# Kernel optimization log

Measured on AMD Instinct MI355X. Metric: run time of the kernel, lower is better.

## Reference

```python
import jax, jax.numpy as jnp
import numpy as np

N_EL = 1024
N_UP = 512
D_EMB = 256
WIDTH = 64

def get_all_pair_indices(n_el, n_up):
    # static numpy precompute, identical to the source module
    ii, jj = np.meshgrid(np.arange(n_el), np.arange(n_el), indexing='ij')
    spin = np.concatenate([np.zeros(n_up, dtype=int), np.ones(n_el - n_up, dtype=int)])
    idx = np.stack([ii.flatten(), jj.flatten()], axis=0)
    idx = idx[:, idx[0] != idx[1]]
    same = spin[idx[0]] == spin[idx[1]]
    return idx[:, same], idx[:, ~same]

_PAIRS = get_all_pair_indices(N_EL, N_UP)

def logscaled_diff_features(diff):
    # [P,3] diff -> [P,4]: log-rescaled diff vector + log1p(distance)
    r = jnp.linalg.norm(diff, axis=-1, keepdims=True)
    return jnp.concatenate([diff * jnp.log1p(r) / r, jnp.log1p(r)], axis=-1)

def mlp3(x, W0, b0, W1, b1, W2, b2=None):
    h = jnp.tanh(x @ W0 + b0)
    h = jnp.tanh(h @ W1 + b1)
    out = h @ W2
    return out if b2 is None else out + b2

def _forward(electrons, embeddings, A_same, A_diff, Ws0_same, bs0_same, Ws1_same, bs1_same, Ws2_same, Ws0_diff, bs0_diff, Ws1_diff, bs1_diff, Ws2_diff, scale_same, scale_diff, We0, be0, We1, be1, We2, be2, mlp_scale, log_bias):
    (ics, ins_), (icd, ind_) = _PAIRS
    diff_same = electrons[ics] - electrons[ins_]   # [P_same,3]
    diff_diff = electrons[icd] - electrons[ind_]   # [P_diff,3]
    dist_same = jnp.linalg.norm(diff_same, axis=-1)
    dist_diff = jnp.linalg.norm(diff_diff, axis=-1)
    # Yukawa e-e cusp
    A_s = jax.nn.softplus(A_same); F_s = jnp.sqrt(2 * A_s)
    A_d = jax.nn.softplus(A_diff); F_d = jnp.sqrt(2 * A_d)
    logpsi = A_s * jnp.sum(jnp.expm1(-dist_same / F_s) / dist_same)
    logpsi = logpsi + A_d * jnp.sum(jnp.expm1(-dist_diff / F_d) / dist_diff)
    # pairwise e-e MLPs
    fs = logscaled_diff_features(diff_same)
    fd = logscaled_diff_features(diff_diff)
    logpsi = logpsi + jnp.sum(mlp3(fs, Ws0_same, bs0_same, Ws1_same, bs1_same, Ws2_same)) * scale_same
    logpsi = logpsi + jnp.sum(mlp3(fd, Ws0_diff, bs0_diff, Ws1_diff, bs1_diff, Ws2_diff)) * scale_diff
    # per-electron embedding MLP jastrow
    J = mlp3(embeddings, We0, be0, We1, be1, We2, be2) * mlp_scale  # [n_el, 2]
    J = J + jnp.stack([jnp.zeros(()), log_bias])
    jastrows = J.sum(axis=0)  # (2,)
    log_J = jastrows[1]
    sign = jnp.sign(log_J)
    logpsi = logpsi + jastrows[0] + jnp.log(jnp.abs(log_J))
    return sign, logpsi

def setup_inputs():
    key = jax.random.key(0)
    ks = jax.random.split(key, 16)
    rn = lambda k, s: jax.random.normal(k, s, dtype=jnp.float32)
    return dict(
        electrons=rn(ks[0], (N_EL, 3)),
        embeddings=rn(ks[1], (N_EL, D_EMB)),
        A_same=jnp.ones(()), A_diff=jnp.ones(()),
        Ws0_same=rn(ks[2], (4, WIDTH)) * 0.3, bs0_same=jnp.zeros((WIDTH,)),
        Ws1_same=rn(ks[3], (WIDTH, WIDTH)) * 0.1, bs1_same=jnp.zeros((WIDTH,)),
        Ws2_same=rn(ks[4], (WIDTH, 1)) * 0.1,
        Ws0_diff=rn(ks[5], (4, WIDTH)) * 0.3, bs0_diff=jnp.zeros((WIDTH,)),
        Ws1_diff=rn(ks[6], (WIDTH, WIDTH)) * 0.1, bs1_diff=jnp.zeros((WIDTH,)),
        Ws2_diff=rn(ks[7], (WIDTH, 1)) * 0.1,
        scale_same=rn(ks[8], ()) * 0.1, scale_diff=rn(ks[9], ()) * 0.1,
        We0=rn(ks[10], (D_EMB, WIDTH)) * 0.05, be0=jnp.zeros((WIDTH,)),
        We1=rn(ks[11], (WIDTH, WIDTH)) * 0.1, be1=jnp.zeros((WIDTH,)),
        We2=rn(ks[12], (WIDTH, 2)) * 0.1, be2=jnp.zeros((2,)),
        mlp_scale=rn(ks[13], (2,)) * 0.1,
        log_bias=jnp.ones(()),
    )

def reference(electrons, embeddings, A_same, A_diff, Ws0_same, bs0_same, Ws1_same, bs1_same, Ws2_same, Ws0_diff, bs0_diff, Ws1_diff, bs1_diff, Ws2_diff, scale_same, scale_diff, We0, be0, We1, be1, We2, be2, mlp_scale, log_bias):
    return _forward(electrons, embeddings, A_same, A_diff, Ws0_same, bs0_same, Ws1_same, bs1_same, Ws2_same, Ws0_diff, bs0_diff, Ws1_diff, bs1_diff, Ws2_diff, scale_same, scale_diff, We0, be0, We1, be1, We2, be2, mlp_scale, log_bias)
```

## Files before the change

kernel.cpp:

```cpp
#include <hip/hip_runtime.h>

#define NEL 1024
#define NUP 512
#define DEMB 256
#define WID 64

typedef __attribute__((ext_vector_type(4))) float f32x4;
typedef __attribute__((ext_vector_type(16))) float f32x16;
typedef __attribute__((ext_vector_type(4))) unsigned int u32x4;
typedef __attribute__((ext_vector_type(8))) _Float16 f16x8;
typedef __attribute__((ext_vector_type(2))) _Float16 h2;

#define CTANH 2.8853900817779268f
#define LOG2E 1.4426950408889634f
#define LN2   0.6931471805599453f


__device__ __forceinline__ float tanh_pre(float y) {
    float e = __builtin_amdgcn_exp2f(y);
    return fmaf(-2.0f, __builtin_amdgcn_rcpf(e + 1.0f), 1.0f);
}

__device__ __forceinline__ float softplus_f(float x) {
    return fmaxf(x, 0.0f) + __logf(1.0f + __expf(-fabsf(x)));
}

__device__ __forceinline__ h2 h2s(float f) {
    _Float16 v = (_Float16)f; h2 r; r[0] = v; r[1] = v; return r;
}
__device__ __forceinline__ h2 bch2(unsigned u) { return __builtin_bit_cast(h2, u); }
__device__ __forceinline__ unsigned h2bits(h2 h) { return __builtin_bit_cast(unsigned, h); }

__device__ __forceinline__ h2 tanh2(h2 x) {
    x = __builtin_elementwise_min(h2s(4.0f), __builtin_elementwise_max(h2s(-4.0f), x));
    h2 xq = x * h2s(0.25f);
    h2 v  = xq * xq;
    h2 p  = h2s(-5.150581f);
    p = p * v + h2s(16.252870f);
    p = p * v + h2s(-19.909140f);
    p = p * v + h2s(12.125338f);
    p = p * v + h2s(-4.052176f);
    p = p * v + h2s(0.983638f);
    return x * p;
}

__global__ __launch_bounds__(256) void prep_kernel(
    const float* __restrict__ W0s, const float* __restrict__ b0s,
    const float* __restrict__ W1s, const float* __restrict__ b1s, const float* __restrict__ W2s,
    const float* __restrict__ W0d, const float* __restrict__ b0d,
    const float* __restrict__ W1d, const float* __restrict__ b1d, const float* __restrict__ W2d,
    const float* __restrict__ As, const float* __restrict__ Ad,
    const float* __restrict__ ss, const float* __restrict__ sd,
    float* __restrict__ wsf)
{
    const int b = blockIdx.x, tid = threadIdx.x;
    if (b < 16) {
        const int s = b >> 3, h = (b >> 2) & 1, kc = b & 3;
        const float* W1 = s ? W1d : W1s;
        _Float16* w1out = (_Float16*)(wsf + 2048) + s * 4096 + (h * 4 + kc) * 512;
        #pragma unroll
        for (int it = 0; it < 2; ++it) {
            const int id = tid + it * 256;
            const int l = id >> 3, e = id & 7;
            const int k = kc * 16 + (l >> 5) * 8 + e;
            const int n = h * 32 + (l & 31);
            w1out[id] = (_Float16)W1[k * 64 + n];
        }
    } else {
        for (int idx = tid; idx < 1024; idx += 256) wsf[idx] = 0.0f;
        #pragma unroll
        for (int s = 0; s < 2; ++s) {
            const float* W0 = s ? W0d : W0s;
            const float* b0 = s ? b0d : b0s;
            const float* b1 = s ? b1d : b1s;
            const float* w2 = s ? W2d : W2s;
            const float scl = (s ? sd : ss)[0];
            const int base = 1024 + s * 512;
            if (tid < 64) wsf[base + tid] = b1[tid];
            if (tid < 64) {
                const int h = tid >> 5, hi = (tid >> 4) & 1, rp = (tid >> 1) & 7, wh = tid & 1;
                const int n = h * 32 + ((2 * rp) & 3) + 8 * (rp >> 1) + 4 * hi + wh;
                ((_Float16*)(wsf + base + 64))[tid] = (_Float16)(scl * w2[n]);
            }
            {
                const int kc = tid >> 6, hi = (tid >> 5) & 1, ep = (tid >> 3) & 3;
                const int k = (tid >> 1) & 3, wh = tid & 1;
                const int n = kc * 16 + hi * 8 + 2 * ep + wh;
                ((_Float16*)(wsf + base + 96))[tid] = (_Float16)W0[k * 64 + n];
            }
            if (tid < 64) {
                const int kc = tid >> 4, hi = (tid >> 3) & 1, ep = (tid >> 1) & 3, wh = tid & 1;
                ((_Float16*)(wsf + base + 224))[tid] = (_Float16)b0[kc * 16 + hi * 8 + 2 * ep + wh];
            }
            if (tid == 0) {
                const float A = softplus_f((s ? Ad : As)[0]);
                wsf[base + 256] = A;
                wsf[base + 257] = LOG2E * __builtin_amdgcn_rsqf(2.0f * A);
            }
        }
    }
}

__global__ __launch_bounds__(256, 6) void pair_kernel(
    const float* __restrict__ electrons,
    const float* __restrict__ wsf,
    float* __restrict__ accum)
{
    __shared__ __align__(16) char smem[8592];
    char*  w1lds = smem;
    float* b1sh  = (float*)(smem + 8192);
    char*  w2lds = smem + 8448;
    float* wsum  = (float*)(smem + 8576);

    const int tid  = threadIdx.x;
    const int bidx = blockIdx.x;
    const int i  = bidx >> 3;
    const int jb = (bidx & 7) << 7;
    const int sset = ((i < NUP) == (jb < NUP)) ? 0 : 1;
    const float* tb = wsf + 1024 + sset * 512;

    {
        const float4* src = (const float4*)(wsf + 2048 + sset * 2048);
        float4* dst = (float4*)w1lds;
        dst[tid]       = src[tid];
        dst[tid + 256] = src[tid + 256];
        if (tid < 16) ((float4*)b1sh)[tid] = ((const float4*)tb)[tid];
        if (tid < 8)  ((float4*)w2lds)[tid] = ((const float4*)(tb + 64))[tid];
    }
    const float A     = tb[256];
    const float invF2 = tb[257];

    const int lane = tid & 63, wv = tid >> 6;
    const int hi = lane >> 5, p32 = lane & 31;
    const int j = jb + (wv << 5) + p32;
    const bool diag = (j == i);

    const float eix = electrons[3 * i], eiy = electrons[3 * i + 1], eiz = electrons[3 * i + 2];
    float dx = eix - electrons[3 * j];
    float dy = eiy - electrons[3 * j + 1];
    float dz = eiz - electrons[3 * j + 2];
    if (diag) { dx = 0.0f; dy = 0.0f; dz = 0.0f; }
    float r2 = fmaf(dx, dx, fmaf(dy, dy, dz * dz));
    if (diag) r2 = 1.0f;
    const float rr    = __builtin_amdgcn_sqrtf(r2);
    const float inv_r = __builtin_amdgcn_rcpf(rr);
    const float l1p   = __builtin_amdgcn_logf(1.0f + rr) * LN2;
    const float gf    = l1p * inv_r;
    const float cusp = (hi == 0 && !diag)
        ? A * (__builtin_amdgcn_exp2f(-rr * invF2) - 1.0f) * inv_r : 0.0f;

    const h2 fs0 = h2s(dx * gf);
    const h2 fs1 = h2s(dy * gf);
    const h2 fs2 = h2s(dz * gf);
    const h2 fs3 = h2s(diag ? 0.0f : l1p);

    __syncthreads();

    const char* w0g = (const char*)(tb + 96);
    const char* b0g = (const char*)(tb + 224);
    f16x8 afr[4];
    #pragma unroll
    for (int kc = 0; kc < 4; ++kc) {
        const u32x4 b0v = *(const u32x4*)(b0g + (((kc << 1) + hi) << 4));
        u32x4 frag;
        #pragma unroll
        for (int ep = 0; ep < 4; ++ep) {
            const u32x4 wv4 = *(const u32x4*)(w0g + (((kc << 1) + hi) << 6) + (ep << 4));
            h2 a = bch2(b0v[ep]);
            a = bch2(wv4[0]) * fs0 + a;
            a = bch2(wv4[1]) * fs1 + a;
            a = bch2(wv4[2]) * fs2 + a;
            a = bch2(wv4[3]) * fs3 + a;
            frag[ep] = h2bits(tanh2(a));
        }
        afr[kc] = __builtin_bit_cast(f16x8, frag);
    }

    float ssum = 0.0f;
    #pragma unroll
    for (int h = 0; h < 2; ++h) {
        f32x16 acc;
        #pragma unroll
        for (int q = 0; q < 4; ++q) {
            const f32x4 bv = *(const f32x4*)(b1sh + (h << 5) + (q << 3) + (hi << 2));
            #pragma unroll
            for (int e = 0; e < 4; ++e) acc[(q << 2) + e] = bv[e];
        }
        #pragma unroll
        for (int kc = 0; kc < 4; ++kc) {
            const f16x8 wa = *(const f16x8*)(w1lds + ((((h << 2) + kc) << 6) + lane) * 16);
            acc = __builtin_amdgcn_mfma_f32_32x32x16_f16(wa, afr[kc], acc, 0, 0, 0);
        }
        const char* w2c = w2lds + (((h << 1) + hi) << 5);
        const u32x4 w2a = *(const u32x4*)(w2c);
        const u32x4 w2b = *(const u32x4*)(w2c + 16);
        h2 s2 = h2s(0.0f);
        #pragma unroll
        for (int q = 0; q < 4; ++q) {
            h2 p0; p0[0] = (_Float16)acc[(q << 2) + 0]; p0[1] = (_Float16)acc[(q << 2) + 1];
            h2 p1; p1[0] = (_Float16)acc[(q << 2) + 2]; p1[1] = (_Float16)acc[(q << 2) + 3];
            const h2 t0 = tanh2(p0);
            const h2 t1 = tanh2(p1);
            const unsigned wlo = (q < 2) ? w2a[(q << 1)]     : w2b[((q - 2) << 1)];
            const unsigned whi = (q < 2) ? w2a[(q << 1) + 1] : w2b[((q - 2) << 1) + 1];
            s2 = t0 * bch2(wlo) + s2;
            s2 = t1 * bch2(whi) + s2;
        }
        ssum += (float)s2[0] + (float)s2[1];
    }
    if (diag) ssum = 0.0f;
    float partial = ssum + cusp;

    #pragma unroll
    for (int off = 32; off; off >>= 1) partial += __shfl_down(partial, off);
    if (lane == 0) wsum[wv] = partial;
    __syncthreads();
    if (tid == 0)
        atomicAdd(&accum[(bidx & 63) << 4], wsum[0] + wsum[1] + wsum[2] + wsum[3]);
}

__global__ __launch_bounds__(256) void embed_kernel(
    const float* __restrict__ emb,
    const float* __restrict__ We0, const float* __restrict__ be0,
    const float* __restrict__ We1, const float* __restrict__ be1,
    const float* __restrict__ We2, const float* __restrict__ be2,
    const float* __restrict__ mlp_scale, const float* __restrict__ log_bias,
    float* __restrict__ accum)
{
    __shared__ float xs[DEMB];
    __shared__ float part1[4 * WID];
    __shared__ float h0s[WID];
    __shared__ float part2[4 * WID];
    const int tid = threadIdx.x, wv = tid >> 6, lane = tid & 63;
    const int r = blockIdx.x;

    xs[tid] = emb[(r << 8) + tid];
    __syncthreads();

    const int kb = wv << 6;
    float a0 = 0, a1 = 0, a2 = 0, a3 = 0;
    #pragma unroll
    for (int q = 0; q < 64; q += 4) {
        a0 = fmaf(xs[kb + q],     We0[(kb + q)     * WID + lane], a0);
        a1 = fmaf(xs[kb + q + 1], We0[(kb + q + 1) * WID + lane], a1);
        a2 = fmaf(xs[kb + q + 2], We0[(kb + q + 2) * WID + lane], a2);
        a3 = fmaf(xs[kb + q + 3], We0[(kb + q + 3) * WID + lane], a3);
    }
    part1[(wv << 6) + lane] = (a0 + a1) + (a2 + a3);
    __syncthreads();

    if (wv == 0) {
        const float s = part1[lane] + part1[64 + lane] + part1[128 + lane]
                      + part1[192 + lane] + be0[lane];
        h0s[lane] = tanh_pre(CTANH * s);
    }
    __syncthreads();

    const int kb2 = wv << 4;
    float c0 = 0, c1 = 0;
    #pragma unroll
    for (int q = 0; q < 16; q += 2) {
        c0 = fmaf(h0s[kb2 + q],     We1[(kb2 + q)     * WID + lane], c0);
        c1 = fmaf(h0s[kb2 + q + 1], We1[(kb2 + q + 1) * WID + lane], c1);
    }
    part2[(wv << 6) + lane] = c0 + c1;
    __syncthreads();

    if (wv == 0) {
        const float c = part2[lane] + part2[64 + lane] + part2[128 + lane]
                      + part2[192 + lane] + be1[lane];
        const float h1 = tanh_pre(CTANH * c);
        float p0 = h1 * We2[2 * lane], p1 = h1 * We2[2 * lane + 1];
        #pragma unroll
        for (int off = 32; off; off >>= 1) {
            p0 += __shfl_down(p0, off);
            p1 += __shfl_down(p1, off);
        }
        if (lane == 0) {
            const int b = (r & 63) << 4;
            atomicAdd(&accum[b + 4], (p0 + be2[0]) * mlp_scale[0]);
            atomicAdd(&accum[b + 8], (p1 + be2[1]) * mlp_scale[1] + log_bias[0]);
        }
    }
}

__global__ __launch_bounds__(64) void final_kernel(const float* __restrict__ accum,
                                                   float* __restrict__ out)
{
    const int lane = threadIdx.x;
    float v  = accum[(lane << 4)];
    float j0 = accum[(lane << 4) + 4];
    float j1 = accum[(lane << 4) + 8];
    #pragma unroll
    for (int off = 32; off; off >>= 1) {
        v  += __shfl_down(v, off);
        j0 += __shfl_down(j0, off);
        j1 += __shfl_down(j1, off);
    }
    if (lane == 0) {
        const float sign = (j1 > 0.0f) ? 1.0f : ((j1 < 0.0f) ? -1.0f : 0.0f);
        out[0] = sign;
        out[1] = v + j0 + logf(fabsf(j1));
    }
}

extern "C" void kernel_launch(void* const* d_in, const int* in_sizes, int n_in,
                              void* d_out, int out_size, void* d_ws, size_t ws_size,
                              hipStream_t stream) {
    const float* electrons  = (const float*)d_in[0];
    const float* embeddings = (const float*)d_in[1];
    const float* A_same     = (const float*)d_in[2];
    const float* A_diff     = (const float*)d_in[3];
    const float* Ws0_same   = (const float*)d_in[4];
    const float* bs0_same   = (const float*)d_in[5];
    const float* Ws1_same   = (const float*)d_in[6];
    const float* bs1_same   = (const float*)d_in[7];
    const float* Ws2_same   = (const float*)d_in[8];
    const float* Ws0_diff   = (const float*)d_in[9];
    const float* bs0_diff   = (const float*)d_in[10];
    const float* bs1w_diff  = (const float*)d_in[11];
    const float* bs1_diff   = (const float*)d_in[12];
    const float* Ws2_diff   = (const float*)d_in[13];
    const float* scale_same = (const float*)d_in[14];
    const float* scale_diff = (const float*)d_in[15];
    const float* We0        = (const float*)d_in[16];
    const float* be0        = (const float*)d_in[17];
    const float* We1        = (const float*)d_in[18];
    const float* be1        = (const float*)d_in[19];
    const float* We2        = (const float*)d_in[20];
    const float* be2        = (const float*)d_in[21];
    const float* mlp_scale  = (const float*)d_in[22];
    const float* log_bias   = (const float*)d_in[23];

    float* out = (float*)d_out;
    float* wsf = (float*)d_ws;

    hipLaunchKernelGGL(prep_kernel, dim3(17), dim3(256), 0, stream,
        Ws0_same, bs0_same, Ws1_same, bs1_same, Ws2_same,
        Ws0_diff, bs0_diff, bs1w_diff, bs1_diff, Ws2_diff,
        A_same, A_diff, scale_same, scale_diff, wsf);

    hipLaunchKernelGGL(pair_kernel, dim3(NEL * NEL / 128), dim3(256), 0, stream,
        electrons, wsf, wsf);

    hipLaunchKernelGGL(embed_kernel, dim3(NEL), dim3(256), 0, stream,
        embeddings, We0, be0, We1, be1, We2, be2, mlp_scale, log_bias, wsf);

    hipLaunchKernelGGL(final_kernel, dim3(1), dim3(64), 0, stream, wsf, out);
}
```

Baseline: 49.87 us.

## Hold W1 fragments in registers, drop LDS staging and block barriers

```diff
diff --git a/kernel.cpp b/kernel.cpp
--- a/kernel.cpp
+++ b/kernel.cpp
@@ -31,17 +31,16 @@
 __device__ __forceinline__ h2 bch2(unsigned u) { return __builtin_bit_cast(h2, u); }
 __device__ __forceinline__ unsigned h2bits(h2 h) { return __builtin_bit_cast(unsigned, h); }
 
-__device__ __forceinline__ h2 tanh2(h2 x) {
-    x = __builtin_elementwise_min(h2s(4.0f), __builtin_elementwise_max(h2s(-4.0f), x));
-    h2 xq = x * h2s(0.25f);
-    h2 v  = xq * xq;
-    h2 p  = h2s(-5.150581f);
+__device__ __forceinline__ h2 tanh2p(h2 u) {
+    u = __builtin_elementwise_min(h2s(1.0f), __builtin_elementwise_max(h2s(-1.0f), u));
+    h2 v = u * u;
+    h2 p = h2s(-5.150581f);
     p = p * v + h2s(16.252870f);
     p = p * v + h2s(-19.909140f);
     p = p * v + h2s(12.125338f);
     p = p * v + h2s(-4.052176f);
     p = p * v + h2s(0.983638f);
-    return x * p;
+    return u * p;
 }
 
 __global__ __launch_bounds__(256) void prep_kernel(
@@ -76,21 +75,21 @@
             const float* w2 = s ? W2d : W2s;
             const float scl = (s ? sd : ss)[0];
             const int base = 1024 + s * 512;
-            if (tid < 64) wsf[base + tid] = b1[tid];
+            if (tid < 64) wsf[base + tid] = 0.25f * b1[tid];
             if (tid < 64) {
                 const int h = tid >> 5, hi = (tid >> 4) & 1, rp = (tid >> 1) & 7, wh = tid & 1;
                 const int n = h * 32 + ((2 * rp) & 3) + 8 * (rp >> 1) + 4 * hi + wh;
-                ((_Float16*)(wsf + base + 64))[tid] = (_Float16)(scl * w2[n]);
+                ((_Float16*)(wsf + base + 64))[tid] = (_Float16)(4.0f * scl * w2[n]);
             }
             {
                 const int kc = tid >> 6, hi = (tid >> 5) & 1, ep = (tid >> 3) & 3;
                 const int k = (tid >> 1) & 3, wh = tid & 1;
                 const int n = kc * 16 + hi * 8 + 2 * ep + wh;
-                ((_Float16*)(wsf + base + 96))[tid] = (_Float16)W0[k * 64 + n];
+                ((_Float16*)(wsf + base + 96))[tid] = (_Float16)(0.25f * W0[k * 64 + n]);
             }
             if (tid < 64) {
                 const int kc = tid >> 4, hi = (tid >> 3) & 1, ep = (tid >> 1) & 3, wh = tid & 1;
-                ((_Float16*)(wsf + base + 224))[tid] = (_Float16)b0[kc * 16 + hi * 8 + 2 * ep + wh];
+                ((_Float16*)(wsf + base + 224))[tid] = (_Float16)(0.25f * b0[kc * 16 + hi * 8 + 2 * ep + wh]);
             }
             if (tid == 0) {
                 const float A = softplus_f((s ? Ad : As)[0]);
@@ -101,39 +100,27 @@
     }
 }
 
-__global__ __launch_bounds__(256, 6) void pair_kernel(
+__global__ __launch_bounds__(256, 4) void pair_kernel(
     const float* __restrict__ electrons,
     const float* __restrict__ wsf,
     float* __restrict__ accum)
 {
-    __shared__ __align__(16) char smem[8592];
-    char*  w1lds = smem;
-    float* b1sh  = (float*)(smem + 8192);
-    char*  w2lds = smem + 8448;
-    float* wsum  = (float*)(smem + 8576);
-
-    const int tid  = threadIdx.x;
-    const int bidx = blockIdx.x;
+    const int tid = threadIdx.x, bidx = blockIdx.x;
+    const int lane = tid & 63, wv = tid >> 6;
     const int i  = bidx >> 3;
-    const int jb = (bidx & 7) << 7;
+    const int jb = ((bidx & 7) << 7) + (wv << 5);
     const int sset = ((i < NUP) == (jb < NUP)) ? 0 : 1;
     const float* tb = wsf + 1024 + sset * 512;
-
-    {
-        const float4* src = (const float4*)(wsf + 2048 + sset * 2048);
-        float4* dst = (float4*)w1lds;
-        dst[tid]       = src[tid];
-        dst[tid + 256] = src[tid + 256];
-        if (tid < 16) ((float4*)b1sh)[tid] = ((const float4*)tb)[tid];
-        if (tid < 8)  ((float4*)w2lds)[tid] = ((const float4*)(tb + 64))[tid];
-    }
-    const float A     = tb[256];
-    const float invF2 = tb[257];
-
-    const int lane = tid & 63, wv = tid >> 6;
+    const char* w1g = (const char*)(wsf + 2048 + sset * 2048);
+
     const int hi = lane >> 5, p32 = lane & 31;
-    const int j = jb + (wv << 5) + p32;
+    const int j = jb + p32;
     const bool diag = (j == i);
+
+    f16x8 wfr[8];
+    #pragma unroll
+    for (int m = 0; m < 8; ++m)
+        wfr[m] = *(const f16x8*)(w1g + (((m << 6) + lane) << 4));
 
     const float eix = electrons[3 * i], eiy = electrons[3 * i + 1], eiz = electrons[3 * i + 2];
     float dx = eix - electrons[3 * j];
@@ -146,6 +133,8 @@
     const float inv_r = __builtin_amdgcn_rcpf(rr);
     const float l1p   = __builtin_amdgcn_logf(1.0f + rr) * LN2;
     const float gf    = l1p * inv_r;
+    const float A     = tb[256];
+    const float invF2 = tb[257];
     const float cusp = (hi == 0 && !diag)
         ? A * (__builtin_amdgcn_exp2f(-rr * invF2) - 1.0f) * inv_r : 0.0f;
 
@@ -153,8 +142,6 @@
     const h2 fs1 = h2s(dy * gf);
     const h2 fs2 = h2s(dz * gf);
     const h2 fs3 = h2s(diag ? 0.0f : l1p);
-
-    __syncthreads();
 
     const char* w0g = (const char*)(tb + 96);
     const char* b0g = (const char*)(tb + 224);
@@ -171,7 +158,7 @@
             a = bch2(wv4[1]) * fs1 + a;
             a = bch2(wv4[2]) * fs2 + a;
             a = bch2(wv4[3]) * fs3 + a;
-            frag[ep] = h2bits(tanh2(a));
+            frag[ep] = h2bits(tanh2p(a));
         }
         afr[kc] = __builtin_bit_cast(f16x8, frag);
     }
@@ -182,25 +169,24 @@
         f32x16 acc;
         #pragma unroll
         for (int q = 0; q < 4; ++q) {
-            const f32x4 bv = *(const f32x4*)(b1sh + (h << 5) + (q << 3) + (hi << 2));
+            const f32x4 bv = *(const f32x4*)(tb + (h << 5) + (q << 3) + (hi << 2));
             #pragma unroll
             for (int e = 0; e < 4; ++e) acc[(q << 2) + e] = bv[e];
         }
         #pragma unroll
-        for (int kc = 0; kc < 4; ++kc) {
-            const f16x8 wa = *(const f16x8*)(w1lds + ((((h << 2) + kc) << 6) + lane) * 16);
-            acc = __builtin_amdgcn_mfma_f32_32x32x16_f16(wa, afr[kc], acc, 0, 0, 0);
-        }
-        const char* w2c = w2lds + (((h << 1) + hi) << 5);
+        for (int kc = 0; kc < 4; ++kc)
+            acc = __builtin_amdgcn_mfma_f32_32x32x16_f16(wfr[(h << 2) + kc], afr[kc], acc, 0, 0, 0);
+
+        const char* w2c = (const char*)(tb + 64) + (((h << 1) + hi) << 5);
         const u32x4 w2a = *(const u32x4*)(w2c);
         const u32x4 w2b = *(const u32x4*)(w2c + 16);
         h2 s2 = h2s(0.0f);
         #pragma unroll
         for (int q = 0; q < 4; ++q) {
-            h2 p0; p0[0] = (_Float16)acc[(q << 2) + 0]; p0[1] = (_Float16)acc[(q << 2) + 1];
-            h2 p1; p1[0] = (_Float16)acc[(q << 2) + 2]; p1[1] = (_Float16)acc[(q << 2) + 3];
-            const h2 t0 = tanh2(p0);
-            const h2 t1 = tanh2(p1);
+            const h2 t0 = tanh2p(__builtin_bit_cast(h2,
+                __builtin_amdgcn_cvt_pkrtz(acc[(q << 2) + 0], acc[(q << 2) + 1])));
+            const h2 t1 = tanh2p(__builtin_bit_cast(h2,
+                __builtin_amdgcn_cvt_pkrtz(acc[(q << 2) + 2], acc[(q << 2) + 3])));
             const unsigned wlo = (q < 2) ? w2a[(q << 1)]     : w2b[((q - 2) << 1)];
             const unsigned whi = (q < 2) ? w2a[(q << 1) + 1] : w2b[((q - 2) << 1) + 1];
             s2 = t0 * bch2(wlo) + s2;
@@ -213,10 +199,8 @@
 
     #pragma unroll
     for (int off = 32; off; off >>= 1) partial += __shfl_down(partial, off);
-    if (lane == 0) wsum[wv] = partial;
-    __syncthreads();
-    if (tid == 0)
-        atomicAdd(&accum[(bidx & 63) << 4], wsum[0] + wsum[1] + wsum[2] + wsum[3]);
+    if (lane == 0)
+        atomicAdd(&accum[(((bidx << 2) + wv) & 63) << 4], partial);
 }
 
 __global__ __launch_bounds__(256) void embed_kernel(
@@ -318,7 +302,7 @@
     const float* Ws2_same   = (const float*)d_in[8];
     const float* Ws0_diff   = (const float*)d_in[9];
     const float* bs0_diff   = (const float*)d_in[10];
-    const float* bs1w_diff  = (const float*)d_in[11];
+    const float* Ws1_diff   = (const float*)d_in[11];
     const float* bs1_diff   = (const float*)d_in[12];
     const float* Ws2_diff   = (const float*)d_in[13];
     const float* scale_same = (const float*)d_in[14];
@@ -337,7 +321,7 @@
 
     hipLaunchKernelGGL(prep_kernel, dim3(17), dim3(256), 0, stream,
         Ws0_same, bs0_same, Ws1_same, bs1_same, Ws2_same,
-        Ws0_diff, bs0_diff, bs1w_diff, bs1_diff, Ws2_diff,
+        Ws0_diff, bs0_diff, Ws1_diff, bs1_diff, Ws2_diff,
         A_same, A_diff, scale_same, scale_diff, wsf);
 
     hipLaunchKernelGGL(pair_kernel, dim3(NEL * NEL / 128), dim3(256), 0, stream,
```

After: 59.90 us. +20.1%, slower.
